# Kernel optimization log

Hardware: AMD Instinct MI355X
Metric: run time of the kernel (lower is better)

## Reference

```python
import jax, jax.numpy as jnp
import numpy as np

B, Q, K = 16, 64, 1024
QS = KS = VS = 256
H = 128
NEG = -1e6


def setup_inputs() -> dict:
    key = jax.random.key(0)
    ks = jax.random.split(key, 7)
    queries = jax.random.normal(ks[0], (B, Q, QS), dtype=jnp.float32)
    keys = jax.random.normal(ks[1], (B, K, KS), dtype=jnp.float32)
    values = jax.random.normal(ks[2], (B, K, VS), dtype=jnp.float32)
    valid_len = jax.random.randint(ks[3], (B,), 0, 512, dtype=jnp.int64)
    # Linear weights (PyTorch Linear stores (out, in); we store (in, out) for x @ W)
    Wq = jax.random.normal(ks[4], (QS, H), dtype=jnp.float32) / np.sqrt(QS)
    Wk = jax.random.normal(ks[5], (KS, H), dtype=jnp.float32) / np.sqrt(KS)
    Ws = jax.random.normal(ks[6], (H,), dtype=jnp.float32) / np.sqrt(H)
    return {"queries": queries, "keys": keys, "values": values,
            "valid_len": valid_len, "Wq": Wq, "Wk": Wk, "Ws": Ws}


def reference(queries, keys, values, valid_len, Wq, Wk, Ws):
    q = jnp.einsum('bqe,eh->bqh', queries, Wq)          # (B,Q,H)
    k = jnp.einsum('bke,eh->bkh', keys, Wk)             # (B,K,H)
    features = jnp.tanh(q[:, :, None, :] + k[:, None, :, :])  # (B,Q,K,H)
    scores = jnp.einsum('bqkh,h->bqk', features, Ws)    # (B,Q,K)
    # front_mask=True: mask the FIRST valid_len[b] key positions
    pos = jnp.arange(K)
    valid = pos[None, None, :] >= valid_len[:, None, None]  # (B,1,K)
    scores = jnp.where(valid, scores, NEG)
    attn = jax.nn.softmax(scores, axis=-1)              # (B,Q,K)
    return jnp.einsum('bqk,bkv->bqv', attn, values)     # (B,Q,VS)
```

## Files before the change

### kernel.cpp

```cpp
#include <hip/hip_runtime.h>

#define NB 16
#define NQ 64
#define NK 1024
#define ES 256
#define NH 128
#define VS 256
#define SCALE2 2.885390081777927f
#define L2E    1.4426950408889634f

__device__ __forceinline__ float exp2_fast(float x) {
    float r; asm("v_exp_f32 %0, %1" : "=v"(r) : "v"(x)); return r;
}
__device__ __forceinline__ float rcp_fast(float x) {
    float r; asm("v_rcp_f32 %0, %1" : "=v"(r) : "v"(x)); return r;
}
__device__ __forceinline__ void fma4(float4& acc, const float4& wv, float s) {
    acc.x = fmaf(wv.x, s, acc.x);
    acc.y = fmaf(wv.y, s, acc.y);
    acc.z = fmaf(wv.z, s, acc.z);
    acc.w = fmaf(wv.w, s, acc.w);
}

__global__ __launch_bounds__(256) void proj_kernel(
    const float* __restrict__ queries, const float* __restrict__ keys,
    const float* __restrict__ Wq, const float* __restrict__ Wk,
    float* __restrict__ qp, float* __restrict__ kp)
{
    __shared__ __align__(16) float x_lds[32 * 256];
    const int bi  = blockIdx.x;
    const int tid = threadIdx.x;

    const float* src; const float* W; float* dst;
    if (bi < 32) {
        src = queries + (size_t)bi * 32 * ES;
        W   = Wq;
        dst = qp + (size_t)bi * 32 * NH;
    } else {
        const int r0 = (bi - 32) * 32;
        src = keys + (size_t)r0 * ES;
        W   = Wk;
        dst = kp + (size_t)r0 * NH;
    }

    const float4* s4 = (const float4*)src;
    float4* x4 = (float4*)x_lds;
#pragma unroll
    for (int i = 0; i < 8; ++i) x4[tid + i * 256] = s4[tid + i * 256];
    __syncthreads();

    const int h4 = tid & 31;
    const int g  = tid >> 5;
    const float* x0 = x_lds + (g +  0) * 256;
    const float* x1 = x_lds + (g +  8) * 256;
    const float* x2 = x_lds + (g + 16) * 256;
    const float* x3 = x_lds + (g + 24) * 256;

    float4 a0 = {0,0,0,0}, a1 = {0,0,0,0}, a2 = {0,0,0,0}, a3 = {0,0,0,0};
#pragma unroll 4
    for (int e = 0; e < 256; e += 4) {
        const float4 v0 = *(const float4*)(x0 + e);
        const float4 v1 = *(const float4*)(x1 + e);
        const float4 v2 = *(const float4*)(x2 + e);
        const float4 v3 = *(const float4*)(x3 + e);
#pragma unroll
        for (int j = 0; j < 4; ++j) {
            const float4 w4 = *(const float4*)(W + (size_t)(e + j) * NH + h4 * 4);
            const float f0 = (j==0)?v0.x:(j==1)?v0.y:(j==2)?v0.z:v0.w;
            const float f1 = (j==0)?v1.x:(j==1)?v1.y:(j==2)?v1.z:v1.w;
            const float f2 = (j==0)?v2.x:(j==1)?v2.y:(j==2)?v2.z:v2.w;
            const float f3 = (j==0)?v3.x:(j==1)?v3.y:(j==2)?v3.z:v3.w;
            fma4(a0, w4, f0); fma4(a1, w4, f1);
            fma4(a2, w4, f2); fma4(a3, w4, f3);
        }
    }
    const float c = SCALE2;
    float4 o;
    o.x=a0.x*c; o.y=a0.y*c; o.z=a0.z*c; o.w=a0.w*c;
    *(float4*)(dst + (size_t)(g +  0) * NH + h4 * 4) = o;
    o.x=a1.x*c; o.y=a1.y*c; o.z=a1.z*c; o.w=a1.w*c;
    *(float4*)(dst + (size_t)(g +  8) * NH + h4 * 4) = o;
    o.x=a2.x*c; o.y=a2.y*c; o.z=a2.z*c; o.w=a2.w*c;
    *(float4*)(dst + (size_t)(g + 16) * NH + h4 * 4) = o;
    o.x=a3.x*c; o.y=a3.y*c; o.z=a3.z*c; o.w=a3.w*c;
    *(float4*)(dst + (size_t)(g + 24) * NH + h4 * 4) = o;
}

__global__ __launch_bounds__(256, 4) void scores_kernel(
    const float* __restrict__ qp, const float* __restrict__ kp,
    const float* __restrict__ Ws, const int* __restrict__ valid_len,
    float* __restrict__ pT)
{
    __shared__ __align__(16) float kp_s[64 * 128];
    __shared__ __align__(16) float qp_s[8 * 128];
    __shared__ __align__(16) float ws_s[128];

    const int kt  = blockIdx.x;
    const int qt  = blockIdx.y;
    const int b   = blockIdx.z;
    const int tid = threadIdx.x;

    const float4* ksrc = (const float4*)(kp + (size_t)(b * NK + kt * 64) * NH);
#pragma unroll
    for (int i = 0; i < 8; ++i) {
        const int idx = tid + i * 256;
        const int row = idx >> 5, c = idx & 31;
        const float4 v = ksrc[idx];
        *(float4*)(kp_s + row * 128 + 4 * (c ^ (row & 7))) = v;
    }
    ((float4*)qp_s)[tid & 255] = ((const float4*)(qp + (size_t)(b * NQ + qt * 8) * NH))[tid & 255];
    if (tid < 32) {
        float4 t = ((const float4*)Ws)[tid];
        t.x *= -2.f; t.y *= -2.f; t.z *= -2.f; t.w *= -2.f;
        ((float4*)ws_s)[tid] = t;
    }
    __syncthreads();

    const int lane = tid & 63;
    const int w    = tid >> 6;

    float sw = ws_s[lane] + ws_s[lane + 64];
#pragma unroll
    for (int off = 32; off; off >>= 1) sw += __shfl_xor(sw, off);
    const float sW = -0.5f * sw;

    const float* qa = qp_s + w * 128;
    const float* qb = qp_s + (w + 4) * 128;
    const float* kr = kp_s + lane * 128;
    const int sw_x = lane & 7;

    float s0 = 0.f, s1 = 0.f;
#pragma unroll 4
    for (int c = 0; c < 32; ++c) {
        const float4 kv = *(const float4*)(kr + 4 * (c ^ sw_x));
        const float4 va = *(const float4*)(qa + 4 * c);
        const float4 vb = *(const float4*)(qb + 4 * c);
        const float4 wv = *(const float4*)(ws_s + 4 * c);
        s0 = fmaf(wv.x, rcp_fast(1.0f + exp2_fast(va.x + kv.x)), s0);
        s0 = fmaf(wv.y, rcp_fast(1.0f + exp2_fast(va.y + kv.y)), s0);
        s0 = fmaf(wv.z, rcp_fast(1.0f + exp2_fast(va.z + kv.z)), s0);
        s0 = fmaf(wv.w, rcp_fast(1.0f + exp2_fast(va.w + kv.w)), s0);
        s1 = fmaf(wv.x, rcp_fast(1.0f + exp2_fast(vb.x + kv.x)), s1);
        s1 = fmaf(wv.y, rcp_fast(1.0f + exp2_fast(vb.y + kv.y)), s1);
        s1 = fmaf(wv.z, rcp_fast(1.0f + exp2_fast(vb.z + kv.z)), s1);
        s1 = fmaf(wv.w, rcp_fast(1.0f + exp2_fast(vb.w + kv.w)), s1);
    }

    const int vl = valid_len[b];
    const int kg = kt * 64 + lane;
    const float p0 = (kg >= vl) ? exp2_fast((sW + s0) * L2E) : 0.0f;
    const float p1 = (kg >= vl) ? exp2_fast((sW + s1) * L2E) : 0.0f;
    pT[((size_t)b * NK + kg) * NQ + qt * 8 + w]     = p0;
    pT[((size_t)b * NK + kg) * NQ + qt * 8 + w + 4] = p1;
}

__global__ __launch_bounds__(256) void pv_kernel(
    const float* __restrict__ pT, const float* __restrict__ values,
    float* __restrict__ part, float* __restrict__ zpart)
{
    __shared__ __align__(16) float a_s[128][36];
    __shared__ float zp_s[4][32];
    const int kt  = blockIdx.x;
    const int qh  = blockIdx.y;
    const int b   = blockIdx.z;
    const int tid = threadIdx.x;

    {
        const int q4 = (tid & 7) * 4;
        const int k0 = tid >> 3;
#pragma unroll
        for (int i = 0; i < 4; ++i) {
            const int k = k0 + 32 * i;
            const float4 v = *(const float4*)(
                pT + ((size_t)b * NK + kt * 128 + k) * NQ + qh * 32 + q4);
            *(float4*)(&a_s[k][q4]) = v;
        }
    }
    __syncthreads();

    {
        const int lane = tid & 63;
        const int w    = tid >> 6;
        const int qq   = lane & 31;
        float z = 0.f;
#pragma unroll
        for (int i = 0; i < 32; ++i) z += a_s[w * 32 + i][qq];
        if (lane < 32) zp_s[w][qq] = z;
    }
    __syncthreads();
    if (tid < 32) {
        const float zf = zp_s[0][tid] + zp_s[1][tid] + zp_s[2][tid] + zp_s[3][tid];
        zpart[((size_t)kt * NB + b) * NQ + qh * 32 + tid] = zf;
    }

    float acc[32];
#pragma unroll
    for (int i = 0; i < 32; ++i) acc[i] = 0.f;

    const float* vb = values + ((size_t)b * NK + kt * 128) * VS + tid;
#pragma unroll 4
    for (int k = 0; k < 128; ++k) {
        const float v = vb[(size_t)k * VS];
#pragma unroll
        for (int j = 0; j < 8; ++j) {
            const float4 a = *(const float4*)(&a_s[k][4 * j]);
            acc[4*j+0] = fmaf(a.x, v, acc[4*j+0]);
            acc[4*j+1] = fmaf(a.y, v, acc[4*j+1]);
            acc[4*j+2] = fmaf(a.z, v, acc[4*j+2]);
            acc[4*j+3] = fmaf(a.w, v, acc[4*j+3]);
        }
    }
#pragma unroll
    for (int q = 0; q < 32; ++q)
        part[(((size_t)kt * NB + b) * NQ + qh * 32 + q) * VS + tid] = acc[q];
}

__global__ __launch_bounds__(256) void finish_kernel(
    const float* __restrict__ part, const float* __restrict__ zpart,
    float* __restrict__ out)
{
    const int r   = blockIdx.x;
    const int tid = threadIdx.x;
    const int b = r >> 6, q = r & 63;
    float z = 0.f, s = 0.f;
#pragma unroll
    for (int kt = 0; kt < 8; ++kt) {
        z += zpart[((size_t)kt * NB + b) * NQ + q];
        s += part[(((size_t)kt * NB + b) * NQ + q) * VS + tid];
    }
    out[(size_t)r * VS + tid] = s / z;
}

extern "C" void kernel_launch(void* const* d_in, const int* in_sizes, int n_in,
                              void* d_out, int out_size, void* d_ws, size_t ws_size,
                              hipStream_t stream)
{
    (void)in_sizes; (void)n_in; (void)out_size; (void)ws_size;
    const float* queries = (const float*)d_in[0];
    const float* keys    = (const float*)d_in[1];
    const float* values  = (const float*)d_in[2];
    const int*   vlen    = (const int*)d_in[3];
    const float* Wq      = (const float*)d_in[4];
    const float* Wk      = (const float*)d_in[5];
    const float* Ws      = (const float*)d_in[6];
    float* out = (float*)d_out;

    float* qp    = (float*)d_ws;
    float* kp    = qp + 131072;
    float* part  = kp;
    float* pT    = kp + 2097152;
    float* zpart = pT + 1048576;

    proj_kernel<<<544, 256, 0, stream>>>(queries, keys, Wq, Wk, qp, kp);
    scores_kernel<<<dim3(16, 8, 16), 256, 0, stream>>>(qp, kp, Ws, vlen, pT);
    pv_kernel<<<dim3(8, 2, 16), 256, 0, stream>>>(pT, values, part, zpart);
    finish_kernel<<<1024, 256, 0, stream>>>(part, zpart, out);
}
```

Before: 166.2 us.

## Skip fully masked key tiles and batch four sigmoid reciprocals into one

```diff
diff --git a/kernel.cpp b/kernel.cpp
--- a/kernel.cpp
+++ b/kernel.cpp
@@ -99,6 +99,16 @@
     const int qt  = blockIdx.y;
     const int b   = blockIdx.z;
     const int tid = threadIdx.x;
+    const int lane = tid & 63;
+    const int w    = tid >> 6;
+    const int kg   = kt * 64 + lane;
+    const int vl   = valid_len[b];
+
+    if (kt * 64 + 63 < vl) {
+        pT[((size_t)b * NK + kg) * NQ + qt * 8 + w]     = 0.0f;
+        pT[((size_t)b * NK + kg) * NQ + qt * 8 + w + 4] = 0.0f;
+        return;
+    }
 
     const float4* ksrc = (const float4*)(kp + (size_t)(b * NK + kt * 64) * NH);
 #pragma unroll
@@ -115,9 +125,6 @@
         ((float4*)ws_s)[tid] = t;
     }
     __syncthreads();
-
-    const int lane = tid & 63;
-    const int w    = tid >> 6;
 
     float sw = ws_s[lane] + ws_s[lane + 64];
 #pragma unroll
@@ -136,18 +143,30 @@
         const float4 va = *(const float4*)(qa + 4 * c);
         const float4 vb = *(const float4*)(qb + 4 * c);
         const float4 wv = *(const float4*)(ws_s + 4 * c);
-        s0 = fmaf(wv.x, rcp_fast(1.0f + exp2_fast(va.x + kv.x)), s0);
-        s0 = fmaf(wv.y, rcp_fast(1.0f + exp2_fast(va.y + kv.y)), s0);
-        s0 = fmaf(wv.z, rcp_fast(1.0f + exp2_fast(va.z + kv.z)), s0);
-        s0 = fmaf(wv.w, rcp_fast(1.0f + exp2_fast(va.w + kv.w)), s0);
-        s1 = fmaf(wv.x, rcp_fast(1.0f + exp2_fast(vb.x + kv.x)), s1);
-        s1 = fmaf(wv.y, rcp_fast(1.0f + exp2_fast(vb.y + kv.y)), s1);
-        s1 = fmaf(wv.z, rcp_fast(1.0f + exp2_fast(vb.z + kv.z)), s1);
-        s1 = fmaf(wv.w, rcp_fast(1.0f + exp2_fast(vb.w + kv.w)), s1);
-    }
-
-    const int vl = valid_len[b];
-    const int kg = kt * 64 + lane;
+        {
+            const float u0 = 1.0f + exp2_fast(va.x + kv.x);
+            const float u1 = 1.0f + exp2_fast(va.y + kv.y);
+            const float u2 = 1.0f + exp2_fast(va.z + kv.z);
+            const float u3 = 1.0f + exp2_fast(va.w + kv.w);
+            const float d01 = u0 * u1, d23 = u2 * u3;
+            const float n01 = fmaf(wv.y, u0, wv.x * u1);
+            const float n23 = fmaf(wv.w, u2, wv.z * u3);
+            const float n   = fmaf(n23, d01, n01 * d23);
+            s0 = fmaf(n, rcp_fast(d01 * d23), s0);
+        }
+        {
+            const float u0 = 1.0f + exp2_fast(vb.x + kv.x);
+            const float u1 = 1.0f + exp2_fast(vb.y + kv.y);
+            const float u2 = 1.0f + exp2_fast(vb.z + kv.z);
+            const float u3 = 1.0f + exp2_fast(vb.w + kv.w);
+            const float d01 = u0 * u1, d23 = u2 * u3;
+            const float n01 = fmaf(wv.y, u0, wv.x * u1);
+            const float n23 = fmaf(wv.w, u2, wv.z * u3);
+            const float n   = fmaf(n23, d01, n01 * d23);
+            s1 = fmaf(n, rcp_fast(d01 * d23), s1);
+        }
+    }
+
     const float p0 = (kg >= vl) ? exp2_fast((sW + s0) * L2E) : 0.0f;
     const float p1 = (kg >= vl) ? exp2_fast((sW + s1) * L2E) : 0.0f;
     pT[((size_t)b * NK + kg) * NQ + qt * 8 + w]     = p0;
@@ -156,6 +175,7 @@
 
 __global__ __launch_bounds__(256) void pv_kernel(
     const float* __restrict__ pT, const float* __restrict__ values,
+    const int* __restrict__ valid_len,
     float* __restrict__ part, float* __restrict__ zpart)
 {
     __shared__ __align__(16) float a_s[128][36];
@@ -164,6 +184,15 @@
     const int qh  = blockIdx.y;
     const int b   = blockIdx.z;
     const int tid = threadIdx.x;
+
+    const int vl = valid_len[b];
+    if (kt * 128 + 127 < vl) {
+        if (tid < 32) zpart[((size_t)kt * NB + b) * NQ + qh * 32 + tid] = 0.f;
+#pragma unroll
+        for (int q = 0; q < 32; ++q)
+            part[(((size_t)kt * NB + b) * NQ + qh * 32 + q) * VS + tid] = 0.f;
+        return;
+    }
 
     {
         const int q4 = (tid & 7) * 4;
@@ -253,6 +282,6 @@
 
     proj_kernel<<<544, 256, 0, stream>>>(queries, keys, Wq, Wk, qp, kp);
     scores_kernel<<<dim3(16, 8, 16), 256, 0, stream>>>(qp, kp, Ws, vlen, pT);
-    pv_kernel<<<dim3(8, 2, 16), 256, 0, stream>>>(pT, values, part, zpart);
+    pv_kernel<<<dim3(8, 2, 16), 256, 0, stream>>>(pT, values, vlen, part, zpart);
     finish_kernel<<<1024, 256, 0, stream>>>(part, zpart, out);
 }
```

New measurement: 165.4 us. No clear change (-0.5%).
